# Kernel optimization log

Hardware: AMD Instinct MI355X
Metric: run time of the kernel (lower is better)

Reference implementation:

```python
import math
import jax
import jax.numpy as jnp
import numpy as np

T, B, C, F = 4096, 8, 1024, 128


def setup_inputs() -> dict:
    key = jax.random.key(0)
    ks = jax.random.split(key, 16)
    sc = 0.02
    inp = {
        "x": jax.random.normal(ks[0], (T, B, C), jnp.float32),
        "state": jax.random.normal(ks[1], (B, F, F), jnp.float32),
        "A_w": jax.random.normal(ks[2], (F, C), jnp.float32) * sc,
        "A_b": jax.random.normal(ks[3], (F,), jnp.float32) * sc,
        "B_w": jax.random.normal(ks[4], (F, C), jnp.float32) * sc,
        "B_b": jax.random.normal(ks[5], (F,), jnp.float32) * sc,
        "C_w": jax.random.normal(ks[6], (F, C), jnp.float32) * sc,
        "C_b": jax.random.normal(ks[7], (F,), jnp.float32) * sc,
        "D_w": jax.random.normal(ks[8], (F, C), jnp.float32) * sc,
        "D_b": jax.random.normal(ks[9], (F,), jnp.float32) * sc,
        "I_w": jax.random.normal(ks[10], (F, C), jnp.float32) * sc,
        "I_b": jax.random.normal(ks[11], (F,), jnp.float32) * sc,
        "S_w": jax.random.normal(ks[12], (F, C), jnp.float32) * sc,
        "S_b": jax.random.normal(ks[13], (F,), jnp.float32) * sc,
        "O_w": jax.random.normal(ks[14], (C, F), jnp.float32) * sc,
    }
    return inp


def reference(x, state, A_w, A_b, B_w, B_b, C_w, C_b, D_w, D_b, I_w, I_b, S_w, S_b, O_w):
    # x: [T, B, C], state: [B, F, F]
    awk_safe = jnp.asarray(math.sqrt(F), x.dtype)

    def proj(W, b):
        return jnp.einsum('tbc,fc->tbf', x, W) + b  # [T, B, F]

    a = proj(A_w, A_b)
    b = proj(B_w, B_b)
    c = proj(C_w, C_b)
    d = proj(D_w, D_b)
    i = proj(I_w, I_b)
    s = proj(S_w, S_b)

    def step(st, ins):
        sel, at, bt, ct, dt, it = ins  # each [B, F]
        # st: [B, F, F]
        st = (st * jax.nn.sigmoid(it)[:, None, :]
              + jnp.einsum('bij,bj->bi', st, at)[:, :, None] * bt[:, None, :] / awk_safe
              + ct[:, :, None] * dt[:, None, :])
        out = jnp.einsum('bi,bij->bj', sel, st)  # [B, F]
        return st, out

    state_out, o = jax.lax.scan(step, state, (s, a, b, c, d, i))
    y = jnp.einsum('tbf,cf->tbc', o, O_w)  # O has no bias
    return y, state_out
```

## Files before the change

### kernel.cpp

```cpp
#include <hip/hip_runtime.h>


#define T_DIM 4096
#define B_DIM 8
#define C_DIM 1024
#define F_DIM 128

typedef __attribute__((ext_vector_type(8))) short bf16x8;
typedef __attribute__((ext_vector_type(4))) float f32x4;

__device__ __forceinline__ unsigned short f2bf(float f) {
  unsigned u = __float_as_uint(f);
  u += 0x7fffu + ((u >> 16) & 1u);
  return (unsigned short)(u >> 16);
}
__device__ __forceinline__ float bfu2f(unsigned u) { return __uint_as_float(u << 16); }

__global__ void cvt_kernel(const float* __restrict__ in, unsigned short* __restrict__ out, int n4) {
  int i = blockIdx.x * blockDim.x + threadIdx.x;
  int stride = gridDim.x * blockDim.x;
  for (; i < n4; i += stride) {
    float4 v = ((const float4*)in)[i];
    ushort4 r;
    r.x = f2bf(v.x); r.y = f2bf(v.y); r.z = f2bf(v.z); r.w = f2bf(v.w);
    ((ushort4*)out)[i] = r;
  }
}

__global__ void pack_w_kernel(const float* __restrict__ Aw, const float* __restrict__ Ab,
                              const float* __restrict__ Bw, const float* __restrict__ Bb,
                              const float* __restrict__ Cw, const float* __restrict__ Cb,
                              const float* __restrict__ Dw, const float* __restrict__ Db,
                              const float* __restrict__ Iw, const float* __restrict__ Ib,
                              const float* __restrict__ Sw, const float* __restrict__ Sb,
                              unsigned short* __restrict__ Wall, float* __restrict__ biasAll) {
  const float scaleB = 0.08838834764831845f;
  int idx = blockIdx.x * 256 + threadIdx.x;
  if (idx < 768 * 1024) {
    int row = idx >> 10, c = idx & 1023;
    int slot = row >> 7, rr = row & 127;
    const float* W = slot == 0 ? Aw : slot == 1 ? Bw : slot == 2 ? Cw
                   : slot == 3 ? Dw : slot == 4 ? Iw : Sw;
    float v = W[rr * 1024 + c];
    if (slot == 1) v *= scaleB;
    Wall[idx] = f2bf(v);
  }
  if (idx < 768) {
    int slot = idx >> 7, rr = idx & 127;
    const float* Bv = slot == 0 ? Ab : slot == 1 ? Bb : slot == 2 ? Cb
                    : slot == 3 ? Db : slot == 4 ? Ib : Sb;
    float v = Bv[rr];
    if (slot == 1) v *= scaleB;
    biasAll[idx] = v;
  }
}

__global__ __launch_bounds__(256) void gemm_bt(
    const unsigned short* __restrict__ A,
    const unsigned short* __restrict__ Bm,
    float* __restrict__ Cm,
    const float* __restrict__ bias,
    int M, int N, int K, int sig_lo, int sig_hi) {
  __shared__ unsigned short As[128 * 32];
  __shared__ unsigned short Bs[128 * 32];
  const int tid = threadIdx.x;
  const int m0 = blockIdx.x * 128;
  const int n0 = blockIdx.y * 128;
  const int wv = tid >> 6, ln = tid & 63;
  const int mo = (wv & 1) * 64, no = (wv >> 1) * 64;
  const int lrow = ln & 15, lq = ln >> 4;
  f32x4 acc[4][4] = {};

  for (int kt = 0; kt < K; kt += 32) {
#pragma unroll
    for (int it = 0; it < 2; ++it) {
      int idx = it * 256 + tid;
      int row = idx >> 2, kc = idx & 3;
      *(int4*)&As[row * 32 + kc * 8] = *(const int4*)&A[(size_t)(m0 + row) * K + kt + kc * 8];
      *(int4*)&Bs[row * 32 + kc * 8] = *(const int4*)&Bm[(size_t)(n0 + row) * K + kt + kc * 8];
    }
    __syncthreads();
    bf16x8 af[4], bf[4];
#pragma unroll
    for (int i = 0; i < 4; ++i) {
      af[i] = *(const bf16x8*)&As[(mo + i * 16 + lrow) * 32 + lq * 8];
      bf[i] = *(const bf16x8*)&Bs[(no + i * 16 + lrow) * 32 + lq * 8];
    }
#pragma unroll
    for (int i = 0; i < 4; ++i)
#pragma unroll
      for (int j = 0; j < 4; ++j)
        acc[i][j] = __builtin_amdgcn_mfma_f32_16x16x32_bf16(af[i], bf[j], acc[i][j], 0, 0, 0);
    __syncthreads();
  }

#pragma unroll
  for (int i = 0; i < 4; ++i) {
#pragma unroll
    for (int j = 0; j < 4; ++j) {
      int col = n0 + no + j * 16 + lrow;
      float bv = bias ? bias[col] : 0.0f;
      bool sig = (col >= sig_lo) && (col < sig_hi);
#pragma unroll
      for (int r = 0; r < 4; ++r) {
        int row = m0 + mo + i * 16 + lq * 4 + r;
        float v = acc[i][j][r] + bv;
        if (sig) v = 1.0f / (1.0f + __expf(-v));
        Cm[(size_t)row * N + col] = v;
      }
    }
  }
}

__device__ __forceinline__ float wave_sum64(float x) {
  x += __int_as_float(__builtin_amdgcn_update_dpp(0, __float_as_int(x), 0x111, 0xf, 0xf, false));
  x += __int_as_float(__builtin_amdgcn_update_dpp(0, __float_as_int(x), 0x112, 0xf, 0xf, false));
  x += __int_as_float(__builtin_amdgcn_update_dpp(0, __float_as_int(x), 0x114, 0xf, 0xf, false));
  x += __int_as_float(__builtin_amdgcn_update_dpp(0, __float_as_int(x), 0x118, 0xf, 0xf, false));
  x += __int_as_float(__builtin_amdgcn_update_dpp(0, __float_as_int(x), 0x142, 0xf, 0xf, false));
  x += __int_as_float(__builtin_amdgcn_update_dpp(0, __float_as_int(x), 0x143, 0xf, 0xf, false));
  return __int_as_float(__builtin_amdgcn_readlane(__float_as_int(x), 63));
}

template <int ROWS>
__global__ __launch_bounds__(256) void scan_kernel(
    const float* __restrict__ P,
    const float* __restrict__ state_in,
    unsigned short* __restrict__ o_part,
    float* __restrict__ state_out) {
  const int b = blockIdx.x;
  const int gq = blockIdx.y;
  const int wave = threadIdx.x >> 6;
  const int lane = threadIdx.x & 63;
  const int r0 = gq * (4 * ROWS) + wave * ROWS;
  const int j0 = lane * 2;
  __shared__ float buf[2][4][8][128];

  float2 st[ROWS];
#pragma unroll
  for (int r = 0; r < ROWS; ++r)
    st[r] = *(const float2*)&state_in[((size_t)b * F_DIM + r0 + r) * F_DIM + j0];

  float2 Pa[4], Pb[4], Pd[4], Pg[4];
  float Pc[4][ROWS], Ps[4][ROWS];
#pragma unroll
  for (int k = 0; k < 4; ++k) {
    const float* Pt = P + ((size_t)k * B_DIM + b) * 768;
    Pa[k] = *(const float2*)(Pt + 0 + j0);
    Pb[k] = *(const float2*)(Pt + 128 + j0);
    Pd[k] = *(const float2*)(Pt + 384 + j0);
    Pg[k] = *(const float2*)(Pt + 512 + j0);
    if constexpr (ROWS == 2) {
      float2 v = *(const float2*)(Pt + 256 + r0); Pc[k][0] = v.x; Pc[k][1] = v.y;
      float2 w = *(const float2*)(Pt + 640 + r0); Ps[k][0] = w.x; Ps[k][1] = w.y;
    } else {
      float4 v = *(const float4*)(Pt + 256 + r0);
      Pc[k][0] = v.x; Pc[k][1] = v.y; Pc[k][2] = v.z; Pc[k][3] = v.w;
      float4 w = *(const float4*)(Pt + 640 + r0);
      Ps[k][0] = w.x; Ps[k][1] = w.y; Ps[k][2] = w.z; Ps[k][3] = w.w;
    }
  }

  for (int t8 = 0; t8 < T_DIM; t8 += 8) {
    const int pb = (t8 >> 3) & 1;
#pragma unroll
    for (int k = 0; k < 8; ++k) {
      const int sl = k & 3;
      float2 a2 = Pa[sl], b2 = Pb[sl], d2 = Pd[sl], g2 = Pg[sl];
      float cc[ROWS], ss[ROWS];
#pragma unroll
      for (int r = 0; r < ROWS; ++r) { cc[r] = Pc[sl][r]; ss[r] = Ps[sl][r]; }

      int tl = t8 + k + 4; tl = tl < T_DIM ? tl : T_DIM - 1;
      const float* Pn = P + ((size_t)tl * B_DIM + b) * 768;
      Pa[sl] = *(const float2*)(Pn + 0 + j0);
      Pb[sl] = *(const float2*)(Pn + 128 + j0);
      Pd[sl] = *(const float2*)(Pn + 384 + j0);
      Pg[sl] = *(const float2*)(Pn + 512 + j0);
      if constexpr (ROWS == 2) {
        float2 v = *(const float2*)(Pn + 256 + r0); Pc[sl][0] = v.x; Pc[sl][1] = v.y;
        float2 w = *(const float2*)(Pn + 640 + r0); Ps[sl][0] = w.x; Ps[sl][1] = w.y;
      } else {
        float4 v = *(const float4*)(Pn + 256 + r0);
        Pc[sl][0] = v.x; Pc[sl][1] = v.y; Pc[sl][2] = v.z; Pc[sl][3] = v.w;
        float4 w = *(const float4*)(Pn + 640 + r0);
        Ps[sl][0] = w.x; Ps[sl][1] = w.y; Ps[sl][2] = w.z; Ps[sl][3] = w.w;
      }

      float vr[ROWS];
#pragma unroll
      for (int r = 0; r < ROWS; ++r)
        vr[r] = wave_sum64(st[r].x * a2.x + st[r].y * a2.y);

      float ox = 0.0f, oy = 0.0f;
#pragma unroll
      for (int r = 0; r < ROWS; ++r) {
        st[r].x = st[r].x * g2.x + vr[r] * b2.x + cc[r] * d2.x;
        st[r].y = st[r].y * g2.y + vr[r] * b2.y + cc[r] * d2.y;
        ox += ss[r] * st[r].x;
        oy += ss[r] * st[r].y;
      }
      *(float2*)&buf[pb][wave][k][j0] = make_float2(ox, oy);
    }
    __syncthreads();
#pragma unroll
    for (int h = 0; h < 4; ++h) {
      int it = threadIdx.x + h * 256;
      int k = it >> 7, col = it & 127;
      float s = buf[pb][0][k][col] + buf[pb][1][k][col] +
                buf[pb][2][k][col] + buf[pb][3][k][col];
      o_part[(((size_t)gq * T_DIM + t8 + k) * B_DIM + b) * F_DIM + col] = f2bf(s);
    }
  }

#pragma unroll
  for (int r = 0; r < ROWS; ++r)
    *(float2*)&state_out[((size_t)b * F_DIM + r0 + r) * F_DIM + j0] = st[r];
}

__global__ void reduce_kernel(const unsigned short* __restrict__ o_part,
                              unsigned short* __restrict__ ob, int G) {
  const size_t NEL = (size_t)T_DIM * B_DIM * F_DIM;
  size_t i = ((size_t)blockIdx.x * 256 + threadIdx.x) * 8;
  if (i >= NEL) return;
  float acc[8] = {0, 0, 0, 0, 0, 0, 0, 0};
  for (int g = 0; g < G; ++g) {
    int4 v = *(const int4*)(o_part + (size_t)g * NEL + i);
    unsigned w0 = (unsigned)v.x, w1 = (unsigned)v.y, w2 = (unsigned)v.z, w3 = (unsigned)v.w;
    acc[0] += bfu2f(w0 & 0xffffu); acc[1] += bfu2f(w0 >> 16);
    acc[2] += bfu2f(w1 & 0xffffu); acc[3] += bfu2f(w1 >> 16);
    acc[4] += bfu2f(w2 & 0xffffu); acc[5] += bfu2f(w2 >> 16);
    acc[6] += bfu2f(w3 & 0xffffu); acc[7] += bfu2f(w3 >> 16);
  }
  int4 o;
  o.x = (int)((unsigned)f2bf(acc[0]) | ((unsigned)f2bf(acc[1]) << 16));
  o.y = (int)((unsigned)f2bf(acc[2]) | ((unsigned)f2bf(acc[3]) << 16));
  o.z = (int)((unsigned)f2bf(acc[4]) | ((unsigned)f2bf(acc[5]) << 16));
  o.w = (int)((unsigned)f2bf(acc[6]) | ((unsigned)f2bf(acc[7]) << 16));
  *(int4*)(ob + i) = o;
}

extern "C" void kernel_launch(void* const* d_in, const int* in_sizes, int n_in,
                              void* d_out, int out_size, void* d_ws, size_t ws_size,
                              hipStream_t stream) {
  const float* x  = (const float*)d_in[0];
  const float* st = (const float*)d_in[1];
  const float* Aw = (const float*)d_in[2];
  const float* Ab = (const float*)d_in[3];
  const float* Bw = (const float*)d_in[4];
  const float* Bb = (const float*)d_in[5];
  const float* Cw = (const float*)d_in[6];
  const float* Cb = (const float*)d_in[7];
  const float* Dw = (const float*)d_in[8];
  const float* Db = (const float*)d_in[9];
  const float* Iw = (const float*)d_in[10];
  const float* Ib = (const float*)d_in[11];
  const float* Sw = (const float*)d_in[12];
  const float* Sb = (const float*)d_in[13];
  const float* Ow = (const float*)d_in[14];

  float* y = (float*)d_out;
  float* state_out = y + (size_t)T_DIM * B_DIM * C_DIM;

  char* ws = (char*)d_ws;
  unsigned short* Wall = (unsigned short*)(ws);
  float* biasAll       = (float*)(ws + 1572864);
  unsigned short* Owb  = (unsigned short*)(ws + 1576960);
  float* P             = (float*)(ws + 1839104);
  unsigned short* ob   = (unsigned short*)(ws + 102502400);
  unsigned short* xb   = (unsigned short*)(ws + 110891008);
  unsigned short* o_part = xb;

  const int G = (ws_size >= 245108736u) ? 16 : 8;

  cvt_kernel<<<4096, 256, 0, stream>>>(x, xb, 33554432 / 4);
  pack_w_kernel<<<3072, 256, 0, stream>>>(Aw, Ab, Bw, Bb, Cw, Cb, Dw, Db, Iw, Ib, Sw, Sb,
                                          Wall, biasAll);
  cvt_kernel<<<128, 256, 0, stream>>>(Ow, Owb, 131072 / 4);
  gemm_bt<<<dim3(256, 6), 256, 0, stream>>>(xb, Wall, P, biasAll, 32768, 768, 1024, 512, 640);
  if (G == 16)
    scan_kernel<2><<<dim3(8, 16), 256, 0, stream>>>(P, st, o_part, state_out);
  else
    scan_kernel<4><<<dim3(8, 8), 256, 0, stream>>>(P, st, o_part, state_out);
  reduce_kernel<<<2048, 256, 0, stream>>>(o_part, ob, G);
  gemm_bt<<<dim3(256, 8), 256, 0, stream>>>(ob, Owb, y, nullptr, 32768, 1024, 128, 0, 0);
}
```

Before: 1.249 ms.

## Deepen scan prefetch ring to 8 steps and use LDS-only barrier

```diff
diff --git a/kernel.cpp b/kernel.cpp
--- a/kernel.cpp
+++ b/kernel.cpp
@@ -141,51 +141,44 @@
   for (int r = 0; r < ROWS; ++r)
     st[r] = *(const float2*)&state_in[((size_t)b * F_DIM + r0 + r) * F_DIM + j0];
 
-  float2 Pa[4], Pb[4], Pd[4], Pg[4];
-  float Pc[4][ROWS], Ps[4][ROWS];
-#pragma unroll
-  for (int k = 0; k < 4; ++k) {
-    const float* Pt = P + ((size_t)k * B_DIM + b) * 768;
-    Pa[k] = *(const float2*)(Pt + 0 + j0);
-    Pb[k] = *(const float2*)(Pt + 128 + j0);
-    Pd[k] = *(const float2*)(Pt + 384 + j0);
-    Pg[k] = *(const float2*)(Pt + 512 + j0);
-    if constexpr (ROWS == 2) {
-      float2 v = *(const float2*)(Pt + 256 + r0); Pc[k][0] = v.x; Pc[k][1] = v.y;
-      float2 w = *(const float2*)(Pt + 640 + r0); Ps[k][0] = w.x; Ps[k][1] = w.y;
-    } else {
-      float4 v = *(const float4*)(Pt + 256 + r0);
-      Pc[k][0] = v.x; Pc[k][1] = v.y; Pc[k][2] = v.z; Pc[k][3] = v.w;
-      float4 w = *(const float4*)(Pt + 640 + r0);
-      Ps[k][0] = w.x; Ps[k][1] = w.y; Ps[k][2] = w.z; Ps[k][3] = w.w;
-    }
-  }
+  float2 Pa[8], Pb[8], Pd[8], Pg[8];
+  float Pc[8][ROWS], Ps[8][ROWS];
+  const size_t PSTEP = (size_t)B_DIM * 768;
+  const float* P0 = P + (size_t)b * 768;
+
+#define RING_LOAD(sl, Pt)                                                   \
+  do {                                                                      \
+    Pa[sl] = *(const float2*)((Pt) + 0 + j0);                               \
+    Pb[sl] = *(const float2*)((Pt) + 128 + j0);                             \
+    Pd[sl] = *(const float2*)((Pt) + 384 + j0);                             \
+    Pg[sl] = *(const float2*)((Pt) + 512 + j0);                             \
+    if constexpr (ROWS == 2) {                                              \
+      float2 v_ = *(const float2*)((Pt) + 256 + r0);                        \
+      Pc[sl][0] = v_.x; Pc[sl][1] = v_.y;                                   \
+      float2 w_ = *(const float2*)((Pt) + 640 + r0);                        \
+      Ps[sl][0] = w_.x; Ps[sl][1] = w_.y;                                   \
+    } else {                                                                \
+      float4 v_ = *(const float4*)((Pt) + 256 + r0);                        \
+      Pc[sl][0] = v_.x; Pc[sl][1] = v_.y; Pc[sl][2] = v_.z; Pc[sl][3] = v_.w; \
+      float4 w_ = *(const float4*)((Pt) + 640 + r0);                        \
+      Ps[sl][0] = w_.x; Ps[sl][1] = w_.y; Ps[sl][2] = w_.z; Ps[sl][3] = w_.w; \
+    }                                                                       \
+  } while (0)
+
+#pragma unroll
+  for (int k = 0; k < 8; ++k) RING_LOAD(k, P0 + (size_t)k * PSTEP);
 
   for (int t8 = 0; t8 < T_DIM; t8 += 8) {
     const int pb = (t8 >> 3) & 1;
 #pragma unroll
     for (int k = 0; k < 8; ++k) {
-      const int sl = k & 3;
-      float2 a2 = Pa[sl], b2 = Pb[sl], d2 = Pd[sl], g2 = Pg[sl];
+      float2 a2 = Pa[k], b2 = Pb[k], d2 = Pd[k], g2 = Pg[k];
       float cc[ROWS], ss[ROWS];
 #pragma unroll
-      for (int r = 0; r < ROWS; ++r) { cc[r] = Pc[sl][r]; ss[r] = Ps[sl][r]; }
-
-      int tl = t8 + k + 4; tl = tl < T_DIM ? tl : T_DIM - 1;
-      const float* Pn = P + ((size_t)tl * B_DIM + b) * 768;
-      Pa[sl] = *(const float2*)(Pn + 0 + j0);
-      Pb[sl] = *(const float2*)(Pn + 128 + j0);
-      Pd[sl] = *(const float2*)(Pn + 384 + j0);
-      Pg[sl] = *(const float2*)(Pn + 512 + j0);
-      if constexpr (ROWS == 2) {
-        float2 v = *(const float2*)(Pn + 256 + r0); Pc[sl][0] = v.x; Pc[sl][1] = v.y;
-        float2 w = *(const float2*)(Pn + 640 + r0); Ps[sl][0] = w.x; Ps[sl][1] = w.y;
-      } else {
-        float4 v = *(const float4*)(Pn + 256 + r0);
-        Pc[sl][0] = v.x; Pc[sl][1] = v.y; Pc[sl][2] = v.z; Pc[sl][3] = v.w;
-        float4 w = *(const float4*)(Pn + 640 + r0);
-        Ps[sl][0] = w.x; Ps[sl][1] = w.y; Ps[sl][2] = w.z; Ps[sl][3] = w.w;
-      }
+      for (int r = 0; r < ROWS; ++r) { cc[r] = Pc[k][r]; ss[r] = Ps[k][r]; }
+
+      const float* Pn = P0 + (size_t)(t8 + k + 8) * PSTEP;
+      RING_LOAD(k, Pn);
 
       float vr[ROWS];
 #pragma unroll
@@ -202,16 +195,25 @@
       }
       *(float2*)&buf[pb][wave][k][j0] = make_float2(ox, oy);
     }
-    __syncthreads();
-#pragma unroll
-    for (int h = 0; h < 4; ++h) {
+    asm volatile("s_waitcnt lgkmcnt(0)" ::: "memory");
+    __builtin_amdgcn_s_barrier();
+    asm volatile("" ::: "memory");
+
+#pragma unroll
+    for (int h = 0; h < 2; ++h) {
       int it = threadIdx.x + h * 256;
-      int k = it >> 7, col = it & 127;
-      float s = buf[pb][0][k][col] + buf[pb][1][k][col] +
-                buf[pb][2][k][col] + buf[pb][3][k][col];
-      o_part[(((size_t)gq * T_DIM + t8 + k) * B_DIM + b) * F_DIM + col] = f2bf(s);
-    }
-  }
+      int k = it >> 6, c2 = (it & 63) * 2;
+      float2 s0 = *(const float2*)&buf[pb][0][k][c2];
+      float2 s1 = *(const float2*)&buf[pb][1][k][c2];
+      float2 s2 = *(const float2*)&buf[pb][2][k][c2];
+      float2 s3 = *(const float2*)&buf[pb][3][k][c2];
+      float sx = s0.x + s1.x + s2.x + s3.x;
+      float sy = s0.y + s1.y + s2.y + s3.y;
+      unsigned pk = (unsigned)f2bf(sx) | ((unsigned)f2bf(sy) << 16);
+      *(unsigned*)&o_part[(((size_t)gq * T_DIM + t8 + k) * B_DIM + b) * F_DIM + c2] = pk;
+    }
+  }
+#undef RING_LOAD
 
 #pragma unroll
   for (int r = 0; r < ROWS; ++r)
```

New measurement: 1.372 ms. 1.1x slower.
